# Kernel tuning notes

Hardware: AMD Instinct MI355X
Metric: run time of the kernel (lower is better)

Reference implementation:

```python
import jax, jax.numpy as jnp
from jax import lax
import numpy as np

# 8-neighbor topology from the original module
TOPO = np.array([[0, 1], [1, 1], [1, 0], [1, -1], [0, -1], [-1, -1], [-1, 0], [-1, 1]])
EPS = 1e-5


def conv(x, w, stride=1, pad=0, groups=1):
    # NCHW / OIHW convolution, no bias (module uses bias=False everywhere)
    return lax.conv_general_dilated(
        x, w, (stride, stride), [(pad, pad), (pad, pad)],
        feature_group_count=groups,
        dimension_numbers=('NCHW', 'OIHW', 'NCHW'))


def bn(x, g, b):
    # training-mode BatchNorm2d (batch statistics, biased variance)
    m = jnp.mean(x, axis=(0, 2, 3), keepdims=True)
    v = jnp.var(x, axis=(0, 2, 3), keepdims=True)
    return g[None, :, None, None] * (x - m) * lax.rsqrt(v + EPS) + b[None, :, None, None]


def setup_inputs() -> dict:
    key = jax.random.key(0)
    ks = jax.random.split(key, 12)
    B, D, NC, H, W = 8, 6, 48, 256, 256
    s = 0.1
    w = lambda k, shape: jax.random.normal(k, shape, jnp.float32) * s
    return dict(
        x=jax.random.normal(ks[0], (B, D, H, W), jnp.float32),
        # compenv_conv: Conv(D->NC,1) BN tanh Conv(NC->1,1)
        ce_w1=w(ks[1], (NC, D, 1, 1)), ce_g=jnp.ones(NC), ce_b=jnp.zeros(NC),
        ce_w2=w(ks[2], (1, NC, 1, 1)),
        # merge_change_determinant: funnel(ConvT(10->NC,3) tanh Conv(NC->NC,3) tanh) BN tanh Conv(NC->1,2,s2) sigmoid
        # ConvT stride-1 k3 expressed as pad-2 conv with conv-equivalent kernel
        md_ct=w(ks[3], (NC, 10, 3, 3)), md_c1=w(ks[4], (NC, NC, 3, 3)),
        md_g=jnp.ones(NC), md_b=jnp.zeros(NC), md_c2=w(ks[5], (1, NC, 2, 2)),
        # cell_merge: Conv(D->NC,2,s2,g3) BN tanh funnel(ConvT(NC->NC,3,g3) tanh Conv(NC->D,3,g3) tanh)
        cm_w1=w(ks[6], (NC, D // 3, 2, 2)), cm_g=jnp.ones(NC), cm_b=jnp.zeros(NC),
        cm_ct=w(ks[7], (NC, NC // 3, 3, 3)), cm_c2=w(ks[8], (D, NC // 3, 3, 3)),
        # born: Conv(D->NC,1) BN tanh Conv(NC->D,1)
        bo_w1=w(ks[9], (NC, D, 1, 1)), bo_g=jnp.ones(NC), bo_b=jnp.zeros(NC),
        bo_w2=w(ks[10], (D, NC, 1, 1)),
    )


def reference(x, ce_w1, ce_g, ce_b, ce_w2, md_ct, md_c1, md_g, md_b, md_c2,
              cm_w1, cm_g, cm_b, cm_ct, cm_c2, bo_w1, bo_g, bo_b, bo_w2):
    # ---- compenv: per-direction roll + 1x1conv/BN/tanh/1x1conv (BN stats per direction, as in torch) ----
    env = []
    for k in range(8):
        t = jnp.roll(x, int(TOPO[k, 0]), axis=3)      # roll_right along W
        t = jnp.roll(t, int(-TOPO[k, 1]), axis=2)     # roll_down along H
        h = jnp.tanh(bn(conv(t, ce_w1), ce_g, ce_b))
        env.append(conv(h, ce_w2))                    # [B,1,H,W]
    ENV = jnp.concatenate(env, axis=1)                # [B,8,H,W]

    # ---- merge change determinant ----
    te = jnp.concatenate([x[:, :2], ENV], axis=1)     # [B,10,H,W]
    h = jnp.tanh(conv(te, md_ct, pad=2))              # ConvT k3 s1 == pad-2 conv -> [B,NC,H+2,W+2]
    h = jnp.tanh(conv(h, md_c1))                      # -> [B,NC,H,W]
    h = jnp.tanh(bn(h, md_g, md_b))
    CHANGE = jax.nn.sigmoid(conv(h, md_c2, stride=2))  # [B,1,H/2,W/2]

    # ---- cell merge ----
    h = jnp.tanh(bn(conv(x, cm_w1, stride=2, groups=3), cm_g, cm_b))  # [B,NC,H/2,W/2]
    h = jnp.tanh(conv(h, cm_ct, pad=2, groups=3))
    xm = jnp.tanh(conv(h, cm_c2, groups=3))           # [B,D,H/2,W/2]

    # ---- born + blend ----
    born = conv(jnp.tanh(bn(conv(xm, bo_w1), bo_g, bo_b)), bo_w2)
    out = xm * (1.0 - CHANGE) + CHANGE * born
    out = jnp.concatenate([jax.nn.sigmoid(out[:, :3]), out[:, 3:]], axis=1)
    return out
```

## Files before the change

kernel.cpp:

```cpp
#include <hip/hip_runtime.h>
#include <stdint.h>

typedef unsigned short ushort_t;

#define B8  8
#define D6  6
#define NC  48
#define HH  256
#define WW  256
#define HWp 65536
#define H2  128
#define HW2 16384

__device__ __constant__ int c_T0[8] = {0,1,1,1,0,-1,-1,-1};
__device__ __constant__ int c_T1[8] = {1,1,0,-1,-1,-1,0,1};

__device__ inline float bf2f(ushort_t u){ union{unsigned int i; float f;} w; w.i = ((unsigned int)u)<<16; return w.f; }
__device__ inline ushort_t f2bf(float f){ union{float f; unsigned int i;} w; w.f=f; unsigned int xx=w.i;
  return (ushort_t)((xx + 0x7fffu + ((xx>>16)&1u)) >> 16); }
__device__ inline float tanhf_(float x){ float e=__expf(2.f*x); return 1.f - 2.f/(e+1.f); }
__device__ inline float sigm_(float x){ return 1.f/(1.f+__expf(-x)); }
__device__ inline float ldg_(const void* p, size_t i, int isbf){
  return isbf ? bf2f(((const ushort_t*)p)[i]) : ((const float*)p)[i];
}

typedef short short8 __attribute__((ext_vector_type(8)));
typedef float f4 __attribute__((ext_vector_type(4)));
typedef ushort_t us4 __attribute__((ext_vector_type(4)));
typedef ushort_t us8 __attribute__((ext_vector_type(8)));
union AB { short8 s; us4 h[2]; us8 u; };

__global__ __launch_bounds__(256) void k_detect(const ushort_t* x, float* flag){
  int t=threadIdx.x; int cnt=0;
  for(int i=t;i<4096;i+=256){
    ushort_t u=x[2*i];
    int e=(u>>7)&0xff;
    if(e>=100 && e<=150) cnt++;
  }
  for(int o=32;o;o>>=1) cnt+=__shfl_down(cnt,o,64);
  __shared__ int sh4[4];
  if((t&63)==0) sh4[t>>6]=cnt;
  __syncthreads();
  if(t==0){ int tot=sh4[0]+sh4[1]+sh4[2]+sh4[3]; flag[0] = (tot>=2048)?1.f:0.f; }
}

struct WC { const ushort_t* src[10]; int off[10]; int n[10]; };

__global__ __launch_bounds__(256) void k_wcvt(WC wc, float* dst, const float* dfl){
  int isbf = dfl[0]>0.5f;
  int t = blockIdx.y; int n = wc.n[t]; const ushort_t* s = wc.src[t]; float* d = dst + wc.off[t];
  for(int i = blockIdx.x*256 + threadIdx.x; i < n; i += gridDim.x*256)
    d[i] = isbf ? bf2f(s[i]) : ((const float*)s)[i];
}

__global__ __launch_bounds__(256) void k_wprep(const float* w2src, const float* w1src,
                                               ushort_t* wb2, ushort_t* wb1){
  int t = blockIdx.x*256+threadIdx.x;
  if(t<3456){
    int lane=t&63; int rest=t>>6;
    int ks=rest&1; int g=rest>>1; int tap=g%9; int nt=g/9;
    int oc=nt*16+(lane&15); int icb=ks*32+((lane>>4)*8);
    #pragma unroll
    for(int j=0;j<8;j++){
      int ic=icb+j;
      float v = (ic<48) ? w2src[(oc*48+ic)*9+tap] : 0.f;
      wb2[(size_t)t*8+j]=f2bf(v);
    }
  } else if(t<5184){
    int tt=t-3456; int lane=tt&63; int g=tt>>6; int tap=g%9; int nt=g/9;
    int oc=nt*16+(lane&15); int icb=(lane>>4)*8;
    #pragma unroll
    for(int j=0;j<8;j++){
      int ic=icb+j;
      float v = (ic<10) ? w1src[(oc*10+ic)*9+tap] : 0.f;
      wb1[(size_t)tt*8+j]=f2bf(v);
    }
  }
}

__global__ __launch_bounds__(256) void k_mom(const void* src, const float* dfl, int isbfc,
                                             int sh, int npix, float* out){
  int isbf = dfl ? (dfl[0]>0.5f) : isbfc;
  float vals[27];
  #pragma unroll
  for(int i=0;i<27;i++) vals[i]=0.f;
  int stride = gridDim.x*256;
  int msk = (1<<sh)-1;
  for(int p = blockIdx.x*256+threadIdx.x; p < npix; p += stride){
    int b = p >> sh; int hw = p & msk;
    float v[6];
    #pragma unroll
    for(int d=0; d<6; d++){
      size_t idx = (((size_t)(b*6+d))<<sh) + hw;
      v[d] = ldg_(src, idx, isbf);
    }
    int q=6;
    #pragma unroll
    for(int d=0;d<6;d++){
      vals[d]+=v[d];
      #pragma unroll
      for(int e=d;e<6;e++){ vals[q] += v[d]*v[e]; q++; }
    }
  }
  __shared__ float red[4][27];
  int wid=threadIdx.x>>6, lane=threadIdx.x&63;
  #pragma unroll
  for(int i=0;i<27;i++){
    float v=vals[i];
    for(int o=32;o;o>>=1) v+=__shfl_down(v,o,64);
    if(lane==0) red[wid][i]=v;
  }
  __syncthreads();
  if(threadIdx.x<27)
    atomicAdd(&out[threadIdx.x],
      red[0][threadIdx.x]+red[1][threadIdx.x]+red[2][threadIdx.x]+red[3][threadIdx.x]);
}

__global__ __launch_bounds__(64) void k_msb(const float* mom, const float* W1,
      const void* g, const void* b, const float* dfl, float invN, float* scale, float* bias){
  int c = threadIdx.x; if(c>=NC) return;
  int isbf = dfl[0]>0.5f;
  const int st[6]={0,6,11,15,18,20};
  float wr[6];
  #pragma unroll
  for(int d=0;d<6;d++) wr[d]=W1[c*6+d];
  float mean=0.f;
  #pragma unroll
  for(int d=0;d<6;d++) mean += wr[d]*mom[d];
  mean *= invN;
  float e2=0.f;
  #pragma unroll
  for(int d=0;d<6;d++){
    #pragma unroll
    for(int e=d;e<6;e++){
      float mm = mom[6 + st[d] + (e-d)];
      e2 += wr[d]*wr[e]*((e==d)?1.f:2.f)*mm;
    }
  }
  e2 *= invN;
  float var = e2 - mean*mean;
  float sc = ldg_(g,c,isbf) * rsqrtf(var + 1e-5f);
  scale[c]=sc; bias[c]= ldg_(b,c,isbf) - sc*mean;
}

__global__ __launch_bounds__(256) void k_env(const void* x, const float* dfl,
      const float* w1, const float* w2, const float* sc, const float* bi, float* e){
  int isbf = dfl[0]>0.5f;
  int p = blockIdx.x*256+threadIdx.x;
  int b = p >> 16; int hw = p & 65535;
  float v[6];
  #pragma unroll
  for(int d=0; d<6; d++) v[d]=ldg_(x,(size_t)(b*6+d)*HWp + hw, isbf);
  float acc=0.f;
  for(int c=0;c<NC;c++){
    float y=0.f;
    #pragma unroll
    for(int d=0;d<6;d++) y += w1[c*6+d]*v[d];
    acc += w2[c]*tanhf_(sc[c]*y + bi[c]);
  }
  e[(size_t)b*HWp + hw]=acc;
}

__global__ __launch_bounds__(256,3) void k_md(const void* x, const float* dfl, const float* e,
      const ushort_t* wb1, const ushort_t* wb2, ushort_t* h2h, float* stats){
  __shared__ __attribute__((aligned(16))) ushort_t te[6400];
  __shared__ __attribute__((aligned(16))) ushort_t h1t[18816];
  __shared__ float red[4][3][16][2];
  int isbf = dfl[0]>0.5f;
  int b = blockIdx.y;
  int ti = blockIdx.x>>4, tj = blockIdx.x&15;
  int i0 = ti*16, j0 = tj*16;
  int lane = threadIdx.x&63, w = threadIdx.x>>6;
  int n = lane&15, quad = lane>>4;
  {
    us8 z;
    #pragma unroll
    for(int j=0;j<8;j++) z[j]=0;
    us8* tp=(us8*)te;
    for(int idx=threadIdx.x; idx<800; idx+=256) tp[idx]=z;
    for(int idx=threadIdx.x; idx<336; idx+=256) *(us8*)&h1t[idx*56+48]=z;
  }
  __syncthreads();
  for(int idx=threadIdx.x; idx<4000; idx+=256){
    int pix = idx/10, ic = idx-pix*10;
    int r = pix/20, c = pix-r*20;
    int gy = i0-2+r, gx = j0-2+c;
    float v = 0.f;
    if(gy>=0 && gy<HH && gx>=0 && gx<WW){
      if(ic<2) v = ldg_(x, ((size_t)(b*6+ic)*HH + gy)*WW + gx, isbf);
      else { int k=ic-2;
        int yy=(gy + c_T1[k]) & 255; int xx=(gx - c_T0[k]) & 255;
        v = e[((size_t)b*HH + yy)*WW + xx]; }
    }
    te[pix*16+ic]=f2bf(v);
  }
  __syncthreads();
  {
    int qoff = (quad&1)*8;
    for(int mt=w; mt<21; mt+=4){
      int p = mt*16 + n;
      int pr = p/18, pc = p-pr*18;
      f4 hacc[3];
      #pragma unroll
      for(int nt=0;nt<3;nt++) hacc[nt]=(f4){0.f,0.f,0.f,0.f};
      #pragma unroll
      for(int tap=0; tap<9; tap++){
        int ki=tap/3, kj=tap%3;
        AB a; a.u = *(const us8*)&te[((pr+ki)*20 + pc+kj)*16 + qoff];
        #pragma unroll
        for(int nt=0;nt<3;nt++){
          AB Bf; Bf.u = *(const us8*)&wb1[((size_t)((nt*9+tap)*64+lane))*8];
          hacc[nt] = __builtin_amdgcn_mfma_f32_16x16x32_bf16(a.s, Bf.s, hacc[nt], 0,0,0);
        }
      }
      int pd = mt*16 + quad*4;
      #pragma unroll
      for(int nt=0;nt<3;nt++){
        #pragma unroll
        for(int r=0;r<4;r++)
          h1t[(pd+r)*56 + nt*16 + n] = f2bf(tanhf_(hacc[nt][r]));
      }
    }
  }
  __syncthreads();
  f4 acc[4][3];
  #pragma unroll
  for(int a=0;a<4;a++)
    #pragma unroll
    for(int c=0;c<3;c++) acc[a][c]=(f4){0.f,0.f,0.f,0.f};
  int q1off = 32 + ((quad<2) ? quad*8 : 16);
  #pragma unroll
  for(int tap=0; tap<9; tap++){
    int ki=tap/3, kj=tap%3;
    AB Bf[3][2];
    #pragma unroll
    for(int nt=0;nt<3;nt++)
      #pragma unroll
      for(int ks=0;ks<2;ks++)
        Bf[nt][ks].u = *(const us8*)&wb2[((size_t)(((nt*9+tap)*2+ks)*64+lane))*8];
    #pragma unroll
    for(int yy=0; yy<4; yy++){
      int y = w*4 + yy;
      int base = ((y+ki)*18 + n + kj)*56;
      AB a0, a1;
      a0.u = *(const us8*)&h1t[base + quad*8];
      a1.u = *(const us8*)&h1t[base + q1off];
      #pragma unroll
      for(int nt=0;nt<3;nt++){
        acc[yy][nt] = __builtin_amdgcn_mfma_f32_16x16x32_bf16(a0.s, Bf[nt][0].s, acc[yy][nt], 0,0,0);
        acc[yy][nt] = __builtin_amdgcn_mfma_f32_16x16x32_bf16(a1.s, Bf[nt][1].s, acc[yy][nt], 0,0,0);
      }
    }
  }
  float s[3]={0.f,0.f,0.f}, q[3]={0.f,0.f,0.f};
  #pragma unroll
  for(int yy=0;yy<4;yy++){
    int Y = i0 + w*4 + yy;
    #pragma unroll
    for(int nt=0;nt<3;nt++){
      int oc = nt*16 + n;
      size_t base = ((size_t)(b*NC+oc)*HH + Y)*WW + j0 + quad*4;
      us4 u;
      #pragma unroll
      for(int r=0;r<4;r++){
        float v=tanhf_(acc[yy][nt][r]);
        u[r]=f2bf(v);
        float vb=bf2f(u[r]);
        s[nt]+=vb; q[nt]+=vb*vb;
      }
      *(us4*)&h2h[base] = u;
    }
  }
  #pragma unroll
  for(int nt=0;nt<3;nt++){
    s[nt]+=__shfl_xor(s[nt],16,64); s[nt]+=__shfl_xor(s[nt],32,64);
    q[nt]+=__shfl_xor(q[nt],16,64); q[nt]+=__shfl_xor(q[nt],32,64);
  }
  if(quad==0){
    #pragma unroll
    for(int nt=0;nt<3;nt++){ red[w][nt][n][0]=s[nt]; red[w][nt][n][1]=q[nt]; }
  }
  __syncthreads();
  if(threadIdx.x<48){
    int oc=threadIdx.x; int nt=oc>>4, nn=oc&15;
    float S=red[0][nt][nn][0]+red[1][nt][nn][0]+red[2][nt][nn][0]+red[3][nt][nn][0];
    float Q=red[0][nt][nn][1]+red[1][nt][nn][1]+red[2][nt][nn][1]+red[3][nt][nn][1];
    atomicAdd(&stats[2*oc],S); atomicAdd(&stats[2*oc+1],Q);
  }
}

__global__ __launch_bounds__(256) void k_cstat(const float* srcf, const ushort_t* srch, int isbf,
      int C, int HWn, int Bn, int S, float* stats){
  int c = blockIdx.x % C; int s = blockIdx.x / C;
  float sum=0.f, sq=0.f;
  for(int b=0;b<Bn;b++){
    size_t base=((size_t)b*C+c)*HWn;
    for(int i=s*256+threadIdx.x; i<HWn; i+=S*256){
      float v = isbf ? bf2f(srch[base+i]) : srcf[base+i];
      sum+=v; sq+=v*v;
    }
  }
  for(int o=32;o;o>>=1){ sum+=__shfl_down(sum,o,64); sq+=__shfl_down(sq,o,64); }
  __shared__ float ls[4], lq[4];
  int wid=threadIdx.x>>6;
  if((threadIdx.x&63)==0){ ls[wid]=sum; lq[wid]=sq; }
  __syncthreads();
  if(threadIdx.x==0){
    atomicAdd(&stats[2*c],   ls[0]+ls[1]+ls[2]+ls[3]);
    atomicAdd(&stats[2*c+1], lq[0]+lq[1]+lq[2]+lq[3]);
  }
}

__global__ __launch_bounds__(64) void k_csb(const float* stats, const void* g, const void* b,
      const float* dfl, float invN, float* scale, float* bias){
  int c=threadIdx.x; if(c>=NC) return;
  int isbf = dfl[0]>0.5f;
  float mean=stats[2*c]*invN; float var=stats[2*c+1]*invN - mean*mean;
  float s=ldg_(g,c,isbf)*rsqrtf(var+1e-5f);
  scale[c]=s; bias[c]=ldg_(b,c,isbf)-s*mean;
}

__global__ __launch_bounds__(256) void k_change(const ushort_t* h2h,
      const float* wc2, const float* sc, const float* bi, float* CH){
  int p=blockIdx.x*256+threadIdx.x;
  int b=p>>14; int rem=p&16383; int i=rem>>7; int j=rem&127;
  float acc=0.f;
  for(int ic=0;ic<NC;ic++){
    size_t base=((size_t)(b*NC+ic)*HH + 2*i)*WW + 2*j;
    float s=sc[ic], t=bi[ic];
    #pragma unroll
    for(int ki=0;ki<2;ki++)
      #pragma unroll
      for(int kj=0;kj<2;kj++){
        float v= bf2f(h2h[base+(size_t)ki*WW+kj]);
        acc += tanhf_(s*v+t)*wc2[ic*4+ki*2+kj];
      }
  }
  CH[p]=sigm_(acc);
}

__global__ __launch_bounds__(256) void k_cm1(const void* x, const float* dfl, const float* w, ushort_t* t1){
  int isbf = dfl[0]>0.5f;
  int p=blockIdx.x*256+threadIdx.x;
  int b=p>>14; int rem=p&16383; int i=rem>>7; int j=rem&127;
  float v[6][2][2];
  #pragma unroll
  for(int d=0;d<6;d++)
    #pragma unroll
    for(int ki=0;ki<2;ki++)
      #pragma unroll
      for(int kj=0;kj<2;kj++)
        v[d][ki][kj]=ldg_(x, ((size_t)(b*6+d)*HH + 2*i+ki)*WW + 2*j+kj, isbf);
  for(int oc=0;oc<NC;oc++){
    int g=oc>>4;
    float a=0.f;
    #pragma unroll
    for(int icl=0;icl<2;icl++)
      #pragma unroll
      for(int ki=0;ki<2;ki++)
        #pragma unroll
        for(int kj=0;kj<2;kj++)
          a += v[2*g+icl][ki][kj]*w[((oc*2+icl)*2+ki)*2+kj];
    t1[((size_t)(b*NC+oc)*HW2) + rem]=f2bf(a);
  }
}

__global__ __launch_bounds__(256) void k_cm2(const ushort_t* t1, const float* sc, const float* bi,
        const float* wct, float* t2){
  __shared__ float as[16][20][21];
  int b=blockIdx.y, g=blockIdx.z;
  int ti=blockIdx.x/9, tj=blockIdx.x%9;
  int i0=ti*16, j0=tj*16;
  int ty=threadIdx.x>>4, tx=threadIdx.x&15;
  for(int idx=threadIdx.x; idx<6400; idx+=256){
    int i=idx/400; int rem=idx-i*400; int r=rem/20; int cc=rem-r*20;
    int cg=g*16+i;
    int y=i0-2+r, xx=j0-2+cc;
    float v=0.f;
    if(y>=0 && y<H2 && xx>=0 && xx<H2)
      v = tanhf_(sc[cg]*bf2f(t1[((size_t)(b*NC+cg)*H2 + y)*H2 + xx]) + bi[cg]);
    as[i][r][cc]=v;
  }
  __syncthreads();
  float acc[16];
  #pragma unroll
  for(int o=0;o<16;o++) acc[o]=0.f;
  for(int i=0;i<16;i++){
    float p[3][3];
    #pragma unroll
    for(int ki=0;ki<3;ki++)
      #pragma unroll
      for(int kj=0;kj<3;kj++) p[ki][kj]=as[i][ty+ki][tx+kj];
    #pragma unroll
    for(int o=0;o<16;o++){
      const float* wp=&wct[((size_t)(g*16+o)*16+i)*9];
      float a=0.f;
      #pragma unroll
      for(int q=0;q<9;q++) a += p[q/3][q%3]*wp[q];
      acc[o]+=a;
    }
  }
  int ii=i0+ty, jj=j0+tx;
  if(ii<130 && jj<130){
    #pragma unroll
    for(int o=0;o<16;o++)
      t2[((size_t)(b*NC+g*16+o)*130 + ii)*130 + jj]=tanhf_(acc[o]);
  }
}

__global__ __launch_bounds__(256) void k_cm3(const float* t2, const float* w, float* xm){
  __shared__ float ts[16][18][20];
  int b=blockIdx.y, g=blockIdx.z;
  int ti=blockIdx.x>>3, tj=blockIdx.x&7;
  int i0=ti*16, j0=tj*16;
  int ty=threadIdx.x>>4, tx=threadIdx.x&15;
  for(int idx=threadIdx.x; idx<16*18*18; idx+=256){
    int i=idx/324; int rem=idx-i*324; int r=rem/18; int cc=rem-r*18;
    int cg=g*16+i;
    ts[i][r][cc]=t2[((size_t)(b*NC+cg)*130 + i0+r)*130 + j0+cc];
  }
  __syncthreads();
  float acc[2]={0.f,0.f};
  for(int icl=0;icl<16;icl++){
    float p[3][3];
    #pragma unroll
    for(int ki=0;ki<3;ki++)
      #pragma unroll
      for(int kj=0;kj<3;kj++) p[ki][kj]=ts[icl][ty+ki][tx+kj];
    #pragma unroll
    for(int ol=0;ol<2;ol++){
      int oc=2*g+ol;
      const float* wp=&w[((size_t)oc*16+icl)*9];
      float a=0.f;
      #pragma unroll
      for(int q=0;q<9;q++) a += p[q/3][q%3]*wp[q];
      acc[ol]+=a;
    }
  }
  int ii=i0+ty, jj=j0+tx;
  #pragma unroll
  for(int ol=0;ol<2;ol++)
    xm[((size_t)(b*6+2*g+ol)*H2 + ii)*H2 + jj]=tanhf_(acc[ol]);
}

__global__ __launch_bounds__(256) void k_final(const float* xm, const float* CH, const float* w1,
      const float* w2, const float* sc, const float* bi, const float* dfl, void* outp){
  int isbf = dfl[0]>0.5f;
  int p=blockIdx.x*256+threadIdx.x;
  int b=p>>14; int rem=p&16383;
  float v[6];
  #pragma unroll
  for(int d=0;d<6;d++) v[d]=xm[((size_t)(b*6+d)*HW2)+rem];
  float born[6]={0.f,0.f,0.f,0.f,0.f,0.f};
  for(int c=0;c<NC;c++){
    float y=0.f;
    #pragma unroll
    for(int d=0;d<6;d++) y+=w1[c*6+d]*v[d];
    float a=tanhf_(sc[c]*y+bi[c]);
    #pragma unroll
    for(int d=0;d<6;d++) born[d]+=w2[d*NC+c]*a;
  }
  float C=CH[p];
  #pragma unroll
  for(int d=0;d<6;d++){
    float o=v[d]*(1.f-C)+C*born[d];
    if(d<3) o=sigm_(o);
    size_t id=((size_t)(b*6+d)*HW2)+rem;
    if(isbf) ((ushort_t*)outp)[id]=f2bf(o); else ((float*)outp)[id]=o;
  }
}

extern "C" void kernel_launch(void* const* d_in, const int* in_sizes, int n_in,
                              void* d_out, int out_size, void* d_ws, size_t ws_size,
                              hipStream_t stream){
  (void)in_sizes; (void)n_in; (void)out_size; (void)ws_size;
  const ushort_t* x    = (const ushort_t*)d_in[0];
  const ushort_t* cew1 = (const ushort_t*)d_in[1];
  const void*     ceg  = d_in[2];
  const void*     ceb  = d_in[3];
  const ushort_t* cew2 = (const ushort_t*)d_in[4];
  const ushort_t* mdct = (const ushort_t*)d_in[5];
  const ushort_t* mdc1 = (const ushort_t*)d_in[6];
  const void*     mdg  = d_in[7];
  const void*     mdb  = d_in[8];
  const ushort_t* mdc2 = (const ushort_t*)d_in[9];
  const ushort_t* cmw1 = (const ushort_t*)d_in[10];
  const void*     cmg  = d_in[11];
  const void*     cmb  = d_in[12];
  const ushort_t* cmct = (const ushort_t*)d_in[13];
  const ushort_t* cmc2 = (const ushort_t*)d_in[14];
  const ushort_t* bow1 = (const ushort_t*)d_in[15];
  const void*     bog  = d_in[16];
  const void*     bob  = d_in[17];
  const ushort_t* bow2 = (const ushort_t*)d_in[18];
  float* ws = (float*)d_ws;

  const long OW_mdct=0, OW_mdc1=4320, OW_cew1=25056, OW_cew2=25344, OW_mdc2=25392,
             OW_cmw1=25584, OW_cmct=25968, OW_cmc2=32880, OW_bow1=33744, OW_bow2=34032;
  const long OFF_STATS=34320;
  const long ST_xmom=OFF_STATS+0,  ST_cesc=OFF_STATS+64,  ST_cebi=OFF_STATS+112,
             ST_h2  =OFF_STATS+160, ST_mdsc=OFF_STATS+256, ST_mdbi=OFF_STATS+304,
             ST_t1  =OFF_STATS+352, ST_cmsc=OFF_STATS+448, ST_cmbi=OFF_STATS+496,
             ST_xmm =OFF_STATS+544, ST_bosc=OFF_STATS+608, ST_bobi=OFF_STATS+656,
             ST_FLAG=OFF_STATS+960;
  const long OFF_WB2 = OFF_STATS + 1024;
  const long OFF_WB1 = OFF_WB2 + 13824;
  const long OFF_E   = OFF_WB1 + 6912;
  const long OFF_H2  = OFF_E + 524288L;
  const long OFF_D   = OFF_H2 + 12582912L;
  const long OFF_T1=OFF_D, OFF_T2=OFF_D+6291456L, OFF_XM=OFF_D+12781056L, OFF_CH=OFF_D+13567488L;

  ushort_t* h2h  = (ushort_t*)(ws + OFF_H2);
  ushort_t* t1h  = (ushort_t*)(ws + OFF_T1);
  ushort_t* wb2  = (ushort_t*)(ws + OFF_WB2);
  ushort_t* wb1  = (ushort_t*)(ws + OFF_WB1);
  const float* dfl = ws + ST_FLAG;

  (void)hipMemsetAsync(ws + OFF_STATS, 0, 1024*sizeof(float), stream);
  hipLaunchKernelGGL(k_detect, dim3(1), 256, 0, stream, x, ws+ST_FLAG);

  WC wc;
  const ushort_t* srcs[10] = {mdct,mdc1,cew1,cew2,mdc2,cmw1,cmct,cmc2,bow1,bow2};
  const int offs[10] = {(int)OW_mdct,(int)OW_mdc1,(int)OW_cew1,(int)OW_cew2,(int)OW_mdc2,
                        (int)OW_cmw1,(int)OW_cmct,(int)OW_cmc2,(int)OW_bow1,(int)OW_bow2};
  const int cnts[10] = {4320,20736,288,48,192,384,6912,864,288,288};
  for(int i=0;i<10;i++){ wc.src[i]=srcs[i]; wc.off[i]=offs[i]; wc.n[i]=cnts[i]; }
  hipLaunchKernelGGL(k_wcvt, dim3(81,10), 256, 0, stream, wc, ws, dfl);
  hipLaunchKernelGGL(k_wprep, dim3(21), 256, 0, stream, ws+OW_mdc1, ws+OW_mdct, wb2, wb1);

  hipLaunchKernelGGL(k_mom, dim3(256), 256, 0, stream, (const void*)x, dfl, 0, 16, B8*HWp, ws+ST_xmom);
  hipLaunchKernelGGL(k_msb, dim3(1), 64, 0, stream, ws+ST_xmom, ws+OW_cew1, ceg, ceb, dfl,
                     1.f/(float)(B8*HWp), ws+ST_cesc, ws+ST_cebi);
  hipLaunchKernelGGL(k_env, dim3(2048), 256, 0, stream, (const void*)x, dfl, ws+OW_cew1, ws+OW_cew2,
                     ws+ST_cesc, ws+ST_cebi, ws+OFF_E);

  hipLaunchKernelGGL(k_md, dim3(256,8), 256, 0, stream, (const void*)x, dfl, ws+OFF_E,
                     wb1, wb2, h2h, ws+ST_h2);
  hipLaunchKernelGGL(k_csb, dim3(1), 64, 0, stream, ws+ST_h2, mdg, mdb, dfl, 1.f/(float)(B8*HWp),
                     ws+ST_mdsc, ws+ST_mdbi);
  hipLaunchKernelGGL(k_change, dim3(512), 256, 0, stream, h2h, ws+OW_mdc2,
                     ws+ST_mdsc, ws+ST_mdbi, ws+OFF_CH);

  hipLaunchKernelGGL(k_cm1, dim3(512), 256, 0, stream, (const void*)x, dfl, ws+OW_cmw1, t1h);
  hipLaunchKernelGGL(k_cstat, dim3(48*8), 256, 0, stream, (const float*)nullptr, t1h, 1,
                     NC, HW2, B8, 8, ws+ST_t1);
  hipLaunchKernelGGL(k_csb, dim3(1), 64, 0, stream, ws+ST_t1, cmg, cmb, dfl, 1.f/(float)(B8*HW2),
                     ws+ST_cmsc, ws+ST_cmbi);
  hipLaunchKernelGGL(k_cm2, dim3(81,8,3), 256, 0, stream, t1h, ws+ST_cmsc, ws+ST_cmbi,
                     ws+OW_cmct, ws+OFF_T2);
  hipLaunchKernelGGL(k_cm3, dim3(64,8,3), 256, 0, stream, ws+OFF_T2, ws+OW_cmc2, ws+OFF_XM);

  hipLaunchKernelGGL(k_mom, dim3(128), 256, 0, stream, (const void*)(ws+OFF_XM), (const float*)nullptr, 0,
                     14, B8*HW2, ws+ST_xmm);
  hipLaunchKernelGGL(k_msb, dim3(1), 64, 0, stream, ws+ST_xmm, ws+OW_bow1, bog, bob, dfl,
                     1.f/(float)(B8*HW2), ws+ST_bosc, ws+ST_bobi);
  hipLaunchKernelGGL(k_final, dim3(512), 256, 0, stream, ws+OFF_XM, ws+OFF_CH, ws+OW_bow1,
                     ws+OW_bow2, ws+ST_bosc, ws+ST_bobi, dfl, d_out);
}
```

Before: 460.6 us.

## Store md activations tile-contiguous, pad LDS stride, parallelize change kernel over channels

```diff
diff --git a/kernel.cpp b/kernel.cpp
--- a/kernel.cpp
+++ b/kernel.cpp
@@ -162,9 +162,9 @@
 }
 
 __global__ __launch_bounds__(256,3) void k_md(const void* x, const float* dfl, const float* e,
-      const ushort_t* wb1, const ushort_t* wb2, ushort_t* h2h, float* stats){
+      const ushort_t* wb1, const ushort_t* wb2, ushort_t* h2t, float* stats){
   __shared__ __attribute__((aligned(16))) ushort_t te[6400];
-  __shared__ __attribute__((aligned(16))) ushort_t h1t[18816];
+  __shared__ __attribute__((aligned(16))) ushort_t h1t[19488];
   __shared__ float red[4][3][16][2];
   int isbf = dfl[0]>0.5f;
   int b = blockIdx.y;
@@ -178,7 +178,7 @@
     for(int j=0;j<8;j++) z[j]=0;
     us8* tp=(us8*)te;
     for(int idx=threadIdx.x; idx<800; idx+=256) tp[idx]=z;
-    for(int idx=threadIdx.x; idx<336; idx+=256) *(us8*)&h1t[idx*56+48]=z;
+    for(int idx=threadIdx.x; idx<336; idx+=256) *(us8*)&h1t[idx*58+48]=z;
   }
   __syncthreads();
   for(int idx=threadIdx.x; idx<4000; idx+=256){
@@ -218,7 +218,7 @@
       for(int nt=0;nt<3;nt++){
         #pragma unroll
         for(int r=0;r<4;r++)
-          h1t[(pd+r)*56 + nt*16 + n] = f2bf(tanhf_(hacc[nt][r]));
+          h1t[(pd+r)*58 + nt*16 + n] = f2bf(tanhf_(hacc[nt][r]));
       }
     }
   }
@@ -241,7 +241,7 @@
     #pragma unroll
     for(int yy=0; yy<4; yy++){
       int y = w*4 + yy;
-      int base = ((y+ki)*18 + n + kj)*56;
+      int base = ((y+ki)*18 + n + kj)*58;
       AB a0, a1;
       a0.u = *(const us8*)&h1t[base + quad*8];
       a1.u = *(const us8*)&h1t[base + q1off];
@@ -253,13 +253,13 @@
     }
   }
   float s[3]={0.f,0.f,0.f}, q[3]={0.f,0.f,0.f};
+  size_t tilebase = ((size_t)(b*256 + blockIdx.x))*48*256;
   #pragma unroll
   for(int yy=0;yy<4;yy++){
-    int Y = i0 + w*4 + yy;
     #pragma unroll
     for(int nt=0;nt<3;nt++){
       int oc = nt*16 + n;
-      size_t base = ((size_t)(b*NC+oc)*HH + Y)*WW + j0 + quad*4;
+      size_t base = tilebase + (size_t)oc*256 + (w*4+yy)*16 + quad*4;
       us4 u;
       #pragma unroll
       for(int r=0;r<4;r++){
@@ -268,7 +268,7 @@
         float vb=bf2f(u[r]);
         s[nt]+=vb; q[nt]+=vb*vb;
       }
-      *(us4*)&h2h[base] = u;
+      *(us4*)&h2t[base] = u;
     }
   }
   #pragma unroll
@@ -320,23 +320,33 @@
   scale[c]=s; bias[c]=ldg_(b,c,isbf)-s*mean;
 }
 
-__global__ __launch_bounds__(256) void k_change(const ushort_t* h2h,
+__global__ __launch_bounds__(256) void k_change(const ushort_t* h2t,
       const float* wc2, const float* sc, const float* bi, float* CH){
-  int p=blockIdx.x*256+threadIdx.x;
-  int b=p>>14; int rem=p&16383; int i=rem>>7; int j=rem&127;
-  float acc=0.f;
-  for(int ic=0;ic<NC;ic++){
-    size_t base=((size_t)(b*NC+ic)*HH + 2*i)*WW + 2*j;
-    float s=sc[ic], t=bi[ic];
-    #pragma unroll
-    for(int ki=0;ki<2;ki++)
-      #pragma unroll
-      for(int kj=0;kj<2;kj++){
-        float v= bf2f(h2h[base+(size_t)ki*WW+kj]);
-        acc += tanhf_(s*v+t)*wc2[ic*4+ki*2+kj];
-      }
-  }
-  CH[p]=sigm_(acc);
+  int tile = blockIdx.x;
+  int b = tile>>8; int rest = tile&255; int ti = rest>>4, tj = rest&15;
+  int t = threadIdx.x;
+  int pix = t&63, icq = t>>6;
+  int oi = pix>>3, oj = pix&7;
+  const ushort_t* tp = &h2t[(size_t)tile*48*256];
+  float acc = 0.f;
+  #pragma unroll
+  for(int icl=0; icl<12; icl++){
+    int ic = icq*12 + icl;
+    float s = sc[ic], tb = bi[ic];
+    const ushort_t* cp = tp + ic*256 + (2*oi)*16 + 2*oj;
+    acc += tanhf_(s*bf2f(cp[0 ])+tb)*wc2[ic*4+0];
+    acc += tanhf_(s*bf2f(cp[1 ])+tb)*wc2[ic*4+1];
+    acc += tanhf_(s*bf2f(cp[16])+tb)*wc2[ic*4+2];
+    acc += tanhf_(s*bf2f(cp[17])+tb)*wc2[ic*4+3];
+  }
+  __shared__ float rr[256];
+  rr[icq*64+pix] = acc;
+  __syncthreads();
+  if(t<64){
+    float v = rr[t]+rr[64+t]+rr[128+t]+rr[192+t];
+    int i = ti*8 + (t>>3), j = tj*8 + (t&7);
+    CH[((size_t)b<<14) + i*128 + j] = sigm_(v);
+  }
 }
 
 __global__ __launch_bounds__(256) void k_cm1(const void* x, const float* dfl, const float* w, ushort_t* t1){
@@ -510,7 +520,7 @@
   const long OFF_D   = OFF_H2 + 12582912L;
   const long OFF_T1=OFF_D, OFF_T2=OFF_D+6291456L, OFF_XM=OFF_D+12781056L, OFF_CH=OFF_D+13567488L;
 
-  ushort_t* h2h  = (ushort_t*)(ws + OFF_H2);
+  ushort_t* h2t  = (ushort_t*)(ws + OFF_H2);
   ushort_t* t1h  = (ushort_t*)(ws + OFF_T1);
   ushort_t* wb2  = (ushort_t*)(ws + OFF_WB2);
   ushort_t* wb1  = (ushort_t*)(ws + OFF_WB1);
@@ -535,10 +545,10 @@
                      ws+ST_cesc, ws+ST_cebi, ws+OFF_E);
 
   hipLaunchKernelGGL(k_md, dim3(256,8), 256, 0, stream, (const void*)x, dfl, ws+OFF_E,
-                     wb1, wb2, h2h, ws+ST_h2);
+                     wb1, wb2, h2t, ws+ST_h2);
   hipLaunchKernelGGL(k_csb, dim3(1), 64, 0, stream, ws+ST_h2, mdg, mdb, dfl, 1.f/(float)(B8*HWp),
                      ws+ST_mdsc, ws+ST_mdbi);
-  hipLaunchKernelGGL(k_change, dim3(512), 256, 0, stream, h2h, ws+OW_mdc2,
+  hipLaunchKernelGGL(k_change, dim3(2048), 256, 0, stream, h2t, ws+OW_mdc2,
                      ws+ST_mdsc, ws+ST_mdbi, ws+OFF_CH);
 
   hipLaunchKernelGGL(k_cm1, dim3(512), 256, 0, stream, (const void*)x, dfl, ws+OW_cmw1, t1h);
```

New measurement: 448.2 us. -2.7%, faster.
